# Performance work log

Hardware: AMD Instinct MI355X
Metric: run time of the kernel (lower is better)

Reference implementation:

```python
import jax, jax.numpy as jnp
import numpy as np

D_MODEL = 1024
N_HEADS = 16
D_HEAD = D_MODEL // N_HEADS
B, T = 4, 2048


def setup_inputs() -> dict:
    key = jax.random.key(0)
    k1, k2, k3 = jax.random.split(key, 3)
    x = jax.random.normal(k1, (B, T, D_MODEL), dtype=jnp.float32)
    # nn.Linear(d_model, 3*d_model, bias=False): y = x @ W_qkv (stored here as [d, 3d])
    W_qkv = jax.random.normal(k2, (D_MODEL, 3 * D_MODEL), dtype=jnp.float32) * (D_MODEL ** -0.5)
    W_out = jax.random.normal(k3, (D_MODEL, D_MODEL), dtype=jnp.float32) * (D_MODEL ** -0.5)
    # causal mask: 1 = keep, 0 = masked (masked_fill(mask == 0, -inf))
    mask = jnp.tril(jnp.ones((T, T), dtype=jnp.int32))
    return {"x": x, "W_qkv": W_qkv, "W_out": W_out, "mask": mask}


def reference(x, W_qkv, W_out, mask):
    Bb, Tt, C = x.shape
    qkv = (x @ W_qkv).reshape(Bb, Tt, 3, N_HEADS, D_HEAD)
    q, k, v = qkv[:, :, 0], qkv[:, :, 1], qkv[:, :, 2]  # each [B,T,H,Dh]
    # scores: [B,H,T,T]
    attn = jnp.einsum('bthd,bshd->bhts', q, k) / jnp.sqrt(jnp.float32(D_HEAD))
    attn = jnp.where(mask == 0, -jnp.inf, attn)
    attn = jax.nn.softmax(attn, axis=-1)
    out = jnp.einsum('bhts,bshd->bthd', attn, v).reshape(Bb, Tt, C)
    return out @ W_out
```

## Files before the change

kernel.cpp:

```cpp
#include <hip/hip_runtime.h>
#include <cstdint>
#include <cstddef>


#define D_MODEL 1024
#define NHEADS  16
#define DHEAD   64
#define BATCH   4
#define SEQ     2048

typedef __attribute__((ext_vector_type(8))) _Float16 half8;
typedef __attribute__((ext_vector_type(4))) _Float16 half4;
typedef __attribute__((ext_vector_type(4))) float    f32x4;

__device__ __forceinline__ void async_copy16(const _Float16* g, _Float16* l) {
    __builtin_amdgcn_global_load_lds(
        (const __attribute__((address_space(1))) uint32_t*)g,
        (__attribute__((address_space(3))) uint32_t*)l, 16, 0, 0);
}

__global__ void cast_f32_f16(const float* __restrict__ in,
                             _Float16* __restrict__ out) {
    int i = blockIdx.x * blockDim.x + threadIdx.x;
    float4 v = *(const float4*)(in + (size_t)i * 4);
    half4 o;
    o.x = (_Float16)v.x; o.y = (_Float16)v.y;
    o.z = (_Float16)v.z; o.w = (_Float16)v.w;
    *(half4*)(out + (size_t)i * 4) = o;
}

__global__ void transpose_cast(const float* __restrict__ in,
                               _Float16* __restrict__ out, int R, int C) {
    __shared__ float tile[32][33];
    int c0 = blockIdx.x * 32, r0 = blockIdx.y * 32;
    int tx = threadIdx.x, ty = threadIdx.y;
    #pragma unroll
    for (int i = 0; i < 32; i += 8)
        tile[ty + i][tx] = in[(size_t)(r0 + ty + i) * C + c0 + tx];
    __syncthreads();
    #pragma unroll
    for (int i = 0; i < 32; i += 8)
        out[(size_t)(c0 + ty + i) * R + r0 + tx] = (_Float16)tile[tx][ty + i];
}

__global__ void gemm_qkv(const _Float16* __restrict__ A,
                         const _Float16* __restrict__ Bt,
                         _Float16* __restrict__ QK,
                         _Float16* __restrict__ Vtg) {
    __shared__ __attribute__((aligned(16))) _Float16 smem[128 * 132];
    _Float16* As = smem;
    _Float16* Bs = smem + 128 * 32;

    const int tid  = threadIdx.x;
    const int w    = tid >> 6, lane = tid & 63;
    const int l15  = lane & 15, quad = lane >> 4;
    const int wm   = w >> 1, wn = w & 1;
    const int row0 = blockIdx.y * 128, col0 = blockIdx.x * 128;
    const int K = 1024;

    f32x4 acc[4][4];
    #pragma unroll
    for (int i = 0; i < 4; i++)
        #pragma unroll
        for (int j = 0; j < 4; j++)
            acc[i][j] = (f32x4){0.f, 0.f, 0.f, 0.f};

    const int r0i = tid >> 2, c0i = tid & 3;
    const int r1i = (256 + tid) >> 2;

    for (int k0 = 0; k0 < K; k0 += 32) {
        __syncthreads();
        async_copy16(A  + (size_t)(row0 + r0i) * K + k0 + c0i * 8, &As[(w * 64) * 8]);
        async_copy16(A  + (size_t)(row0 + r1i) * K + k0 + c0i * 8, &As[(256 + w * 64) * 8]);
        async_copy16(Bt + (size_t)(col0 + r0i) * K + k0 + c0i * 8, &Bs[(w * 64) * 8]);
        async_copy16(Bt + (size_t)(col0 + r1i) * K + k0 + c0i * 8, &Bs[(256 + w * 64) * 8]);
        __syncthreads();

        half8 af[4], bfm[4];
        #pragma unroll
        for (int i = 0; i < 4; i++)
            af[i] = *(const half8*)&As[(wm * 64 + i * 16 + l15) * 32 + quad * 8];
        #pragma unroll
        for (int j = 0; j < 4; j++)
            bfm[j] = *(const half8*)&Bs[(wn * 64 + j * 16 + l15) * 32 + quad * 8];
        #pragma unroll
        for (int i = 0; i < 4; i++)
            #pragma unroll
            for (int j = 0; j < 4; j++)
                acc[i][j] = __builtin_amdgcn_mfma_f32_16x16x32_f16(
                    af[i], bfm[j], acc[i][j], 0, 0, 0);
    }

    if (blockIdx.x < 16) {
        #pragma unroll
        for (int i = 0; i < 4; i++) {
            int row = row0 + wm * 64 + i * 16 + quad * 4;
            #pragma unroll
            for (int j = 0; j < 4; j++) {
                int col = col0 + wn * 64 + j * 16 + l15;
                #pragma unroll
                for (int r = 0; r < 4; r++)
                    QK[(size_t)(row + r) * 2048 + col] = (_Float16)acc[i][j][r];
            }
        }
    } else {
        __syncthreads();
        #pragma unroll
        for (int i = 0; i < 4; i++) {
            int tl = wm * 64 + i * 16 + quad * 4;
            #pragma unroll
            for (int j = 0; j < 4; j++) {
                int vl = wn * 64 + j * 16 + l15;
                half4 pk;
                #pragma unroll
                for (int r = 0; r < 4; r++) pk[r] = (_Float16)acc[i][j][r];
                *(half4*)&smem[vl * 132 + tl] = pk;
            }
        }
        __syncthreads();
        const int bb = row0 >> 11, tb = row0 & 2047;
        const int rr0 = tid >> 4;
        const int cc  = (tid & 15) * 8;
        #pragma unroll
        for (int s = 0; s < 8; s++) {
            int vl = rr0 + s * 16;
            int vcol = (col0 - 2048) + vl;
            int hh = vcol >> 6, d = vcol & 63;
            *(half8*)&Vtg[((size_t)((bb * 16 + hh) * 64 + d)) * 2048 + tb + cc] =
                *(const half8*)&smem[vl * 132 + cc];
        }
    }
}

__global__ void gemm_out(const _Float16* __restrict__ A,
                         const _Float16* __restrict__ Bt,
                         float* __restrict__ Cf, int N, int K) {
    __shared__ __attribute__((aligned(16))) _Float16 As[128 * 32];
    __shared__ __attribute__((aligned(16))) _Float16 Bs[128 * 32];

    const int tid  = threadIdx.x;
    const int w    = tid >> 6, lane = tid & 63;
    const int l15  = lane & 15, quad = lane >> 4;
    const int wm   = w >> 1, wn = w & 1;
    const int row0 = blockIdx.y * 128, col0 = blockIdx.x * 128;

    f32x4 acc[4][4];
    #pragma unroll
    for (int i = 0; i < 4; i++)
        #pragma unroll
        for (int j = 0; j < 4; j++)
            acc[i][j] = (f32x4){0.f, 0.f, 0.f, 0.f};

    const int r0i = tid >> 2, c0i = tid & 3;
    const int r1i = (256 + tid) >> 2;

    for (int k0 = 0; k0 < K; k0 += 32) {
        __syncthreads();
        async_copy16(A  + (size_t)(row0 + r0i) * K + k0 + c0i * 8, &As[(w * 64) * 8]);
        async_copy16(A  + (size_t)(row0 + r1i) * K + k0 + c0i * 8, &As[(256 + w * 64) * 8]);
        async_copy16(Bt + (size_t)(col0 + r0i) * K + k0 + c0i * 8, &Bs[(w * 64) * 8]);
        async_copy16(Bt + (size_t)(col0 + r1i) * K + k0 + c0i * 8, &Bs[(256 + w * 64) * 8]);
        __syncthreads();

        half8 af[4], bfm[4];
        #pragma unroll
        for (int i = 0; i < 4; i++)
            af[i] = *(const half8*)&As[(wm * 64 + i * 16 + l15) * 32 + quad * 8];
        #pragma unroll
        for (int j = 0; j < 4; j++)
            bfm[j] = *(const half8*)&Bs[(wn * 64 + j * 16 + l15) * 32 + quad * 8];
        #pragma unroll
        for (int i = 0; i < 4; i++)
            #pragma unroll
            for (int j = 0; j < 4; j++)
                acc[i][j] = __builtin_amdgcn_mfma_f32_16x16x32_f16(
                    af[i], bfm[j], acc[i][j], 0, 0, 0);
    }

    #pragma unroll
    for (int i = 0; i < 4; i++) {
        int row = row0 + wm * 64 + i * 16 + quad * 4;
        #pragma unroll
        for (int j = 0; j < 4; j++) {
            int col = col0 + wn * 64 + j * 16 + l15;
            #pragma unroll
            for (int r = 0; r < 4; r++)
                Cf[(size_t)(row + r) * N + col] = acc[i][j][r];
        }
    }
}

__global__ __launch_bounds__(256) void flash_attn(
        const _Float16* __restrict__ qk, const _Float16* __restrict__ vt,
        _Float16* __restrict__ obuf) {
    const int pr = blockIdx.x, h = blockIdx.y, b = blockIdx.z;
    const int tid = threadIdx.x;
    const int w = tid >> 6, lane = tid & 63;
    const int l15 = lane & 15, quad = lane >> 4;

    __shared__ __attribute__((aligned(16))) _Float16 Ks[64 * 72];
    __shared__ __attribute__((aligned(16))) _Float16 Vs[64 * 72];
    __shared__ __attribute__((aligned(16))) _Float16 Pl[4][16 * 72];

    const _Float16* kb = qk + (size_t)b * SEQ * 2048 + D_MODEL + h * 64;
    const _Float16* vb = vt + (size_t)(b * 16 + h) * 64 * 2048;

    const int srow = tid >> 3;
    const int sc   = (tid & 7) * 8;

    const float SCL2 = 0.125f * 1.44269504f;
    const float MOFF = 4.0f * 1.44269504f;

    #pragma unroll 1
    for (int phase = 0; phase < 2; ++phase) {
        const int tq = phase ? (31 - pr) : pr;
        const int q0 = tq * 64;
        const int n_iter = tq + 1;

        const _Float16* qp = qk + ((size_t)(b * SEQ + q0 + w * 16 + l15)) * 2048
                             + h * DHEAD + quad * 8;
        half8 qf0 = *(const half8*)qp;
        half8 qf1 = *(const half8*)(qp + 32);

        f32x4 o[4];
        #pragma unroll
        for (int d = 0; d < 4; d++) o[d] = (f32x4){0.f, 0.f, 0.f, 0.f};
        float l_acc = 0.f;

        half8 kr0, kr1, vr0, vr1;
        {
            const _Float16* kp = kb + (size_t)srow * 2048 + sc;
            kr0 = *(const half8*)kp;
            kr1 = *(const half8*)(kp + (size_t)32 * 2048);
            const _Float16* vp = vb + (size_t)srow * 2048 + sc;
            vr0 = *(const half8*)vp;
            vr1 = *(const half8*)(vp + (size_t)32 * 2048);
        }

        #pragma unroll 1
        for (int it = 0; it < n_iter; ++it) {
            __syncthreads();
            *(half8*)&Ks[srow * 72 + sc]        = kr0;
            *(half8*)&Ks[(srow + 32) * 72 + sc] = kr1;
            *(half8*)&Vs[srow * 72 + sc]        = vr0;
            *(half8*)&Vs[(srow + 32) * 72 + sc] = vr1;
            __syncthreads();

            if (it + 1 < n_iter) {
                const int k1 = (it + 1) * 64;
                const _Float16* kp = kb + (size_t)(k1 + srow) * 2048 + sc;
                kr0 = *(const half8*)kp;
                kr1 = *(const half8*)(kp + (size_t)32 * 2048);
                const _Float16* vp = vb + (size_t)srow * 2048 + k1 + sc;
                vr0 = *(const half8*)vp;
                vr1 = *(const half8*)(vp + (size_t)32 * 2048);
            }

            f32x4 st[4];
            #pragma unroll
            for (int nt = 0; nt < 4; nt++) {
                half8 ka0 = *(const half8*)&Ks[(nt * 16 + l15) * 72 + quad * 8];
                half8 ka1 = *(const half8*)&Ks[(nt * 16 + l15) * 72 + 32 + quad * 8];
                f32x4 acc = (f32x4){0.f, 0.f, 0.f, 0.f};
                acc = __builtin_amdgcn_mfma_f32_16x16x32_f16(ka0, qf0, acc, 0, 0, 0);
                acc = __builtin_amdgcn_mfma_f32_16x16x32_f16(ka1, qf1, acc, 0, 0, 0);
                st[nt] = acc;
            }

            if (it == n_iter - 1) {
                #pragma unroll
                for (int nt = 0; nt < 4; nt++)
                    #pragma unroll
                    for (int r = 0; r < 4; r++)
                        st[nt][r] = (nt * 16 + quad * 4 + r <= w * 16 + l15)
                                        ? st[nt][r] * SCL2 - MOFF : -INFINITY;
            } else {
                #pragma unroll
                for (int nt = 0; nt < 4; nt++)
                    #pragma unroll
                    for (int r = 0; r < 4; r++)
                        st[nt][r] = st[nt][r] * SCL2 - MOFF;
            }

            #pragma unroll
            for (int nt = 0; nt < 4; nt++) {
                half4 pk;
                #pragma unroll
                for (int r = 0; r < 4; r++) {
                    float p = exp2f(st[nt][r]);
                    l_acc += p;
                    pk[r] = (_Float16)p;
                }
                *(half4*)&Pl[w][l15 * 72 + nt * 16 + quad * 4] = pk;
            }
            asm volatile("s_waitcnt lgkmcnt(0)" ::: "memory");

            #pragma unroll
            for (int kf = 0; kf < 2; kf++) {
                half8 pf = *(const half8*)&Pl[w][l15 * 72 + kf * 32 + quad * 8];
                #pragma unroll
                for (int dt = 0; dt < 4; dt++) {
                    half8 vf = *(const half8*)&Vs[(dt * 16 + l15) * 72 + kf * 32 + quad * 8];
                    o[dt] = __builtin_amdgcn_mfma_f32_16x16x32_f16(pf, vf, o[dt], 0, 0, 0);
                }
            }
        }

        l_acc += __shfl_xor(l_acc, 16);
        l_acc += __shfl_xor(l_acc, 32);
        float linv[4];
        #pragma unroll
        for (int r = 0; r < 4; r++)
            linv[r] = 1.0f / __shfl(l_acc, quad * 4 + r, 16);

        _Float16* ob = obuf + ((size_t)(b * SEQ + q0 + w * 16 + quad * 4)) * D_MODEL
                       + h * DHEAD;
        #pragma unroll
        for (int r = 0; r < 4; r++) {
            #pragma unroll
            for (int dt = 0; dt < 4; dt++)
                ob[(size_t)r * D_MODEL + dt * 16 + l15] = (_Float16)(o[dt][r] * linv[r]);
        }
    }
}

extern "C" void kernel_launch(void* const* d_in, const int* in_sizes, int n_in,
                              void* d_out, int out_size, void* d_ws, size_t ws_size,
                              hipStream_t stream) {
    const float* x    = (const float*)d_in[0];
    const float* Wqkv = (const float*)d_in[1];
    const float* Wout = (const float*)d_in[2];
    float* out = (float*)d_out;

    char* ws = (char*)d_ws;
    _Float16* Xh   = (_Float16*)(ws);
    _Float16* WqT  = (_Float16*)(ws + ((size_t)16 << 20));
    _Float16* WoT  = (_Float16*)(ws + ((size_t)23 << 20));
    _Float16* QKb  = (_Float16*)(ws + ((size_t)26 << 20));
    _Float16* Vtg  = (_Float16*)(ws + ((size_t)58 << 20));
    _Float16* Obuf = (_Float16*)(ws + ((size_t)74 << 20));

    cast_f32_f16<<<8192, 256, 0, stream>>>(x, Xh);
    transpose_cast<<<dim3(96, 32), dim3(32, 8), 0, stream>>>(Wqkv, WqT, 1024, 3072);
    transpose_cast<<<dim3(32, 32), dim3(32, 8), 0, stream>>>(Wout, WoT, 1024, 1024);
    gemm_qkv<<<dim3(24, 64), 256, 0, stream>>>(Xh, WqT, QKb, Vtg);
    flash_attn<<<dim3(16, NHEADS, BATCH), 256, 0, stream>>>(QKb, Vtg, Obuf);
    gemm_out<<<dim3(8, 64), 256, 0, stream>>>(Obuf, WoT, out, 1024, 1024);
}
```

Before: 299.4 us.

## Double flash-attention query tile to 128 rows per block for K/V reuse

```diff
diff --git a/kernel.cpp b/kernel.cpp
--- a/kernel.cpp
+++ b/kernel.cpp
@@ -190,7 +190,7 @@
     }
 }
 
-__global__ __launch_bounds__(256) void flash_attn(
+__global__ __launch_bounds__(256, 2) void flash_attn(
         const _Float16* __restrict__ qk, const _Float16* __restrict__ vt,
         _Float16* __restrict__ obuf) {
     const int pr = blockIdx.x, h = blockIdx.y, b = blockIdx.z;
@@ -200,7 +200,7 @@
 
     __shared__ __attribute__((aligned(16))) _Float16 Ks[64 * 72];
     __shared__ __attribute__((aligned(16))) _Float16 Vs[64 * 72];
-    __shared__ __attribute__((aligned(16))) _Float16 Pl[4][16 * 72];
+    __shared__ __attribute__((aligned(16))) _Float16 Pl[4][32 * 72];
 
     const _Float16* kb = qk + (size_t)b * SEQ * 2048 + D_MODEL + h * 64;
     const _Float16* vb = vt + (size_t)(b * 16 + h) * 64 * 2048;
@@ -213,19 +213,26 @@
 
     #pragma unroll 1
     for (int phase = 0; phase < 2; ++phase) {
-        const int tq = phase ? (31 - pr) : pr;
-        const int q0 = tq * 64;
-        const int n_iter = tq + 1;
-
-        const _Float16* qp = qk + ((size_t)(b * SEQ + q0 + w * 16 + l15)) * 2048
-                             + h * DHEAD + quad * 8;
-        half8 qf0 = *(const half8*)qp;
-        half8 qf1 = *(const half8*)(qp + 32);
-
-        f32x4 o[4];
-        #pragma unroll
-        for (int d = 0; d < 4; d++) o[d] = (f32x4){0.f, 0.f, 0.f, 0.f};
-        float l_acc = 0.f;
+        const int tq = phase ? (15 - pr) : pr;
+        const int q0 = tq * 128;
+        const int n_iter = 2 * (tq + 1);
+
+        half8 qf[2][2];
+        #pragma unroll
+        for (int g = 0; g < 2; g++) {
+            const _Float16* qp = qk
+                + ((size_t)(b * SEQ + q0 + w * 32 + g * 16 + l15)) * 2048
+                + h * DHEAD + quad * 8;
+            qf[g][0] = *(const half8*)qp;
+            qf[g][1] = *(const half8*)(qp + 32);
+        }
+
+        f32x4 o[2][4];
+        float l_acc[2] = {0.f, 0.f};
+        #pragma unroll
+        for (int g = 0; g < 2; g++)
+            #pragma unroll
+            for (int d = 0; d < 4; d++) o[g][d] = (f32x4){0.f, 0.f, 0.f, 0.f};
 
         half8 kr0, kr1, vr0, vr1;
         {
@@ -256,70 +263,86 @@
                 vr1 = *(const half8*)(vp + (size_t)32 * 2048);
             }
 
-            f32x4 st[4];
+            f32x4 st[2][4];
             #pragma unroll
             for (int nt = 0; nt < 4; nt++) {
                 half8 ka0 = *(const half8*)&Ks[(nt * 16 + l15) * 72 + quad * 8];
                 half8 ka1 = *(const half8*)&Ks[(nt * 16 + l15) * 72 + 32 + quad * 8];
-                f32x4 acc = (f32x4){0.f, 0.f, 0.f, 0.f};
-                acc = __builtin_amdgcn_mfma_f32_16x16x32_f16(ka0, qf0, acc, 0, 0, 0);
-                acc = __builtin_amdgcn_mfma_f32_16x16x32_f16(ka1, qf1, acc, 0, 0, 0);
-                st[nt] = acc;
-            }
-
-            if (it == n_iter - 1) {
-                #pragma unroll
-                for (int nt = 0; nt < 4; nt++)
+                #pragma unroll
+                for (int g = 0; g < 2; g++) {
+                    f32x4 acc = (f32x4){0.f, 0.f, 0.f, 0.f};
+                    acc = __builtin_amdgcn_mfma_f32_16x16x32_f16(ka0, qf[g][0], acc, 0, 0, 0);
+                    acc = __builtin_amdgcn_mfma_f32_16x16x32_f16(ka1, qf[g][1], acc, 0, 0, 0);
+                    st[g][nt] = acc;
+                }
+            }
+
+            #pragma unroll
+            for (int g = 0; g < 2; g++) {
+                const int c0 = __builtin_amdgcn_readfirstlane(
+                    q0 + w * 32 + g * 16 - 64 * it);
+                if (c0 >= 63) {
                     #pragma unroll
-                    for (int r = 0; r < 4; r++)
-                        st[nt][r] = (nt * 16 + quad * 4 + r <= w * 16 + l15)
-                                        ? st[nt][r] * SCL2 - MOFF : -INFINITY;
-            } else {
-                #pragma unroll
-                for (int nt = 0; nt < 4; nt++)
+                    for (int nt = 0; nt < 4; nt++)
+                        #pragma unroll
+                        for (int r = 0; r < 4; r++)
+                            st[g][nt][r] = st[g][nt][r] * SCL2 - MOFF;
+                } else {
                     #pragma unroll
-                    for (int r = 0; r < 4; r++)
-                        st[nt][r] = st[nt][r] * SCL2 - MOFF;
-            }
-
-            #pragma unroll
-            for (int nt = 0; nt < 4; nt++) {
-                half4 pk;
-                #pragma unroll
-                for (int r = 0; r < 4; r++) {
-                    float p = exp2f(st[nt][r]);
-                    l_acc += p;
-                    pk[r] = (_Float16)p;
+                    for (int nt = 0; nt < 4; nt++)
+                        #pragma unroll
+                        for (int r = 0; r < 4; r++)
+                            st[g][nt][r] = (nt * 16 + quad * 4 + r - l15 <= c0)
+                                               ? st[g][nt][r] * SCL2 - MOFF
+                                               : -INFINITY;
                 }
-                *(half4*)&Pl[w][l15 * 72 + nt * 16 + quad * 4] = pk;
+                #pragma unroll
+                for (int nt = 0; nt < 4; nt++) {
+                    half4 pk;
+                    #pragma unroll
+                    for (int r = 0; r < 4; r++) {
+                        float p = exp2f(st[g][nt][r]);
+                        l_acc[g] += p;
+                        pk[r] = (_Float16)p;
+                    }
+                    *(half4*)&Pl[w][(g * 16 + l15) * 72 + nt * 16 + quad * 4] = pk;
+                }
             }
             asm volatile("s_waitcnt lgkmcnt(0)" ::: "memory");
 
             #pragma unroll
             for (int kf = 0; kf < 2; kf++) {
-                half8 pf = *(const half8*)&Pl[w][l15 * 72 + kf * 32 + quad * 8];
+                half8 pf0 = *(const half8*)&Pl[w][l15 * 72 + kf * 32 + quad * 8];
+                half8 pf1 = *(const half8*)&Pl[w][(16 + l15) * 72 + kf * 32 + quad * 8];
                 #pragma unroll
                 for (int dt = 0; dt < 4; dt++) {
                     half8 vf = *(const half8*)&Vs[(dt * 16 + l15) * 72 + kf * 32 + quad * 8];
-                    o[dt] = __builtin_amdgcn_mfma_f32_16x16x32_f16(pf, vf, o[dt], 0, 0, 0);
+                    o[0][dt] = __builtin_amdgcn_mfma_f32_16x16x32_f16(pf0, vf, o[0][dt], 0, 0, 0);
+                    o[1][dt] = __builtin_amdgcn_mfma_f32_16x16x32_f16(pf1, vf, o[1][dt], 0, 0, 0);
                 }
             }
         }
 
-        l_acc += __shfl_xor(l_acc, 16);
-        l_acc += __shfl_xor(l_acc, 32);
-        float linv[4];
-        #pragma unroll
-        for (int r = 0; r < 4; r++)
-            linv[r] = 1.0f / __shfl(l_acc, quad * 4 + r, 16);
-
-        _Float16* ob = obuf + ((size_t)(b * SEQ + q0 + w * 16 + quad * 4)) * D_MODEL
-                       + h * DHEAD;
-        #pragma unroll
-        for (int r = 0; r < 4; r++) {
-            #pragma unroll
-            for (int dt = 0; dt < 4; dt++)
-                ob[(size_t)r * D_MODEL + dt * 16 + l15] = (_Float16)(o[dt][r] * linv[r]);
+        #pragma unroll
+        for (int g = 0; g < 2; g++) {
+            float l = l_acc[g];
+            l += __shfl_xor(l, 16);
+            l += __shfl_xor(l, 32);
+            float linv[4];
+            #pragma unroll
+            for (int r = 0; r < 4; r++)
+                linv[r] = 1.0f / __shfl(l, quad * 4 + r, 16);
+
+            _Float16* ob = obuf
+                + ((size_t)(b * SEQ + q0 + w * 32 + g * 16 + quad * 4)) * D_MODEL
+                + h * DHEAD;
+            #pragma unroll
+            for (int r = 0; r < 4; r++) {
+                #pragma unroll
+                for (int dt = 0; dt < 4; dt++)
+                    ob[(size_t)r * D_MODEL + dt * 16 + l15] =
+                        (_Float16)(o[g][dt][r] * linv[r]);
+            }
         }
     }
 }
@@ -344,6 +367,6 @@
     transpose_cast<<<dim3(96, 32), dim3(32, 8), 0, stream>>>(Wqkv, WqT, 1024, 3072);
     transpose_cast<<<dim3(32, 32), dim3(32, 8), 0, stream>>>(Wout, WoT, 1024, 1024);
     gemm_qkv<<<dim3(24, 64), 256, 0, stream>>>(Xh, WqT, QKb, Vtg);
-    flash_attn<<<dim3(16, NHEADS, BATCH), 256, 0, stream>>>(QKb, Vtg, Obuf);
+    flash_attn<<<dim3(8, NHEADS, BATCH), 256, 0, stream>>>(QKb, Vtg, Obuf);
     gemm_out<<<dim3(8, 64), 256, 0, stream>>>(Obuf, WoT, out, 1024, 1024);
 }
```

Measured after the change: 281.5 us. -6.0%, faster.
